# Kernel optimization log

Measured on AMD Instinct MI355X. Metric: run time of the kernel, lower is better.

## Reference

```python
import jax, jax.numpy as jnp
import numpy as np
from jax import lax

B, C_IN, H, W = 128, 3, 256, 256
C_OUT, K = 16, 3


def setup_inputs() -> dict:
    key = jax.random.key(0)
    k1, k2, k3 = jax.random.split(key, 3)
    x = jax.random.normal(k1, (B, C_IN, H, W), dtype=jnp.float32)
    # PyTorch ConvTranspose2d weight layout: (in_channels, out_channels, kH, kW)
    weight = jax.random.normal(k2, (C_IN, C_OUT, K, K), dtype=jnp.float32) * (1.0 / np.sqrt(C_IN * K * K))
    bias = jax.random.normal(k3, (C_OUT, 1, 1), dtype=jnp.float32)
    return {"x": x, "weight": weight, "bias": bias}


def reference(x, weight, bias):
    # conv_transpose2d(stride=1, padding=0) == full correlation with spatially
    # flipped kernel, with in/out channel axes swapped to OIHW.
    k = weight.shape[-1]
    w = jnp.flip(weight, axis=(2, 3)).transpose(1, 0, 2, 3)  # [C_out, C_in, k, k]
    y = lax.conv_general_dilated(
        x, w,
        window_strides=(1, 1),
        padding=[(k - 1, k - 1), (k - 1, k - 1)],
        dimension_numbers=("NCHW", "OIHW", "NCHW"),
    )  # [B, C_out, H+k-1, W+k-1]
    y = jnp.mean(y, axis=(2, 3), keepdims=True)          # [B, C_out, 1, 1]
    y = y + bias[None]                                   # broadcast [C_out,1,1]
    y = jax.nn.logsumexp(y, axis=1, keepdims=True)       # [B, 1, 1, 1]
    y = jnp.sum(y, axis=(2, 3))                          # [B, 1]
    return y * 10.0
```

## Files before the change

### kernel.cpp

```cpp
#include <hip/hip_runtime.h>

#define BATCH   128
#define C_IN    3
#define C_OUT   16
#define F4_PER_PLANE 16384
#define THREADS 1024
#define NWAVES  (THREADS / 64)
#define NBLK    (BATCH * 2)
#define F4_HALF (F4_PER_PLANE / 2)
#define ITERS   (F4_HALF / THREADS)

#define CNT_OFF 1024
#define CNT_STRIDE 16

__global__ __launch_bounds__(THREADS) void fused_pair(
        const float* __restrict__ x,
        const float* __restrict__ weight,
        const float* __restrict__ bias,
        float* __restrict__ ws,
        float* __restrict__ out) {
    const int b    = blockIdx.x >> 1;
    const int half = blockIdx.x & 1;
    const int t    = threadIdx.x;
    const float4* xp = (const float4*)x
                     + (size_t)b * (3 * F4_PER_PLANE) + half * F4_HALF;

    float a0 = 0.0f, a1 = 0.0f, a2 = 0.0f;
#pragma unroll
    for (int i = 0; i < ITERS; ++i) {
        float4 v0 = xp[0 * F4_PER_PLANE + i * THREADS + t];
        float4 v1 = xp[1 * F4_PER_PLANE + i * THREADS + t];
        float4 v2 = xp[2 * F4_PER_PLANE + i * THREADS + t];
        a0 += (v0.x + v0.y) + (v0.z + v0.w);
        a1 += (v1.x + v1.y) + (v1.z + v1.w);
        a2 += (v2.x + v2.y) + (v2.z + v2.w);
    }

#pragma unroll
    for (int off = 32; off > 0; off >>= 1) {
        a0 += __shfl_down(a0, off, 64);
        a1 += __shfl_down(a1, off, 64);
        a2 += __shfl_down(a2, off, 64);
    }
    __shared__ float smem[NWAVES][3];
    const int lane = t & 63;
    const int wv   = t >> 6;
    if (lane == 0) { smem[wv][0] = a0; smem[wv][1] = a1; smem[wv][2] = a2; }
    __syncthreads();

    if (t != 0) return;

    float S0 = 0.0f, S1 = 0.0f, S2 = 0.0f;
#pragma unroll
    for (int w = 0; w < NWAVES; ++w) {
        S0 += smem[w][0]; S1 += smem[w][1]; S2 += smem[w][2];
    }

    float* slot = ws + blockIdx.x * 4;
    slot[0] = S0; slot[1] = S1; slot[2] = S2;
    __threadfence();
    unsigned* cnt = (unsigned*)(ws + CNT_OFF) + b * CNT_STRIDE;
    unsigned prev = atomicAdd(cnt, 1u);
    if (prev != 1u) return;

    __threadfence();
    const float* pslot = ws + (blockIdx.x ^ 1) * 4;
    S0 += pslot[0]; S1 += pslot[1]; S2 += pslot[2];

    const float inv_area = 1.0f / (258.0f * 258.0f);
    float m[C_OUT];
    float mmax = -1e30f;
#pragma unroll
    for (int co = 0; co < C_OUT; ++co) {
        float v = bias[co];
        float w0 = 0.0f, w1 = 0.0f, w2 = 0.0f;
#pragma unroll
        for (int k = 0; k < 9; ++k) {
            w0 += weight[(0 * C_OUT + co) * 9 + k];
            w1 += weight[(1 * C_OUT + co) * 9 + k];
            w2 += weight[(2 * C_OUT + co) * 9 + k];
        }
        v += (S0 * w0 + S1 * w1 + S2 * w2) * inv_area;
        m[co] = v;
        mmax = fmaxf(mmax, v);
    }
    float se = 0.0f;
#pragma unroll
    for (int co = 0; co < C_OUT; ++co) se += expf(m[co] - mmax);
    out[b] = 10.0f * (logf(se) + mmax);
}

extern "C" void kernel_launch(void* const* d_in, const int* in_sizes, int n_in,
                              void* d_out, int out_size, void* d_ws, size_t ws_size,
                              hipStream_t stream) {
    const float* x      = (const float*)d_in[0];
    const float* weight = (const float*)d_in[1];
    const float* bias   = (const float*)d_in[2];
    float* out = (float*)d_out;
    float* ws  = (float*)d_ws;

    hipMemsetAsync(ws + CNT_OFF, 0, BATCH * CNT_STRIDE * sizeof(unsigned), stream);
    fused_pair<<<NBLK, THREADS, 0, stream>>>(x, weight, bias, ws, out);
}
```

Measured before the change: 160.6 us.

## Split fused reduction into main reduce and separate finalize kernel

After: 148.6 us. 7.5% less time.

```diff
diff --git a/kernel.cpp b/kernel.cpp
--- a/kernel.cpp
+++ b/kernel.cpp
@@ -10,15 +10,9 @@
 #define F4_HALF (F4_PER_PLANE / 2)
 #define ITERS   (F4_HALF / THREADS)
 
-#define CNT_OFF 1024
-#define CNT_STRIDE 16
-
-__global__ __launch_bounds__(THREADS) void fused_pair(
+__global__ __launch_bounds__(THREADS) void main_reduce(
         const float* __restrict__ x,
-        const float* __restrict__ weight,
-        const float* __restrict__ bias,
-        float* __restrict__ ws,
-        float* __restrict__ out) {
+        float* __restrict__ part) {
     const int b    = blockIdx.x >> 1;
     const int half = blockIdx.x & 1;
     const int t    = threadIdx.x;
@@ -48,46 +42,52 @@
     if (lane == 0) { smem[wv][0] = a0; smem[wv][1] = a1; smem[wv][2] = a2; }
     __syncthreads();
 
-    if (t != 0) return;
+    if (t == 0) {
+        float S0 = 0.0f, S1 = 0.0f, S2 = 0.0f;
+#pragma unroll
+        for (int w = 0; w < NWAVES; ++w) {
+            S0 += smem[w][0]; S1 += smem[w][1]; S2 += smem[w][2];
+        }
+        float* slot = part + blockIdx.x * 4;
+        slot[0] = S0; slot[1] = S1; slot[2] = S2;
+    }
+}
 
-    float S0 = 0.0f, S1 = 0.0f, S2 = 0.0f;
+__global__ __launch_bounds__(BATCH) void finalize(
+        const float* __restrict__ part,
+        const float* __restrict__ weight,
+        const float* __restrict__ bias,
+        float* __restrict__ out) {
+    __shared__ float Wsum[C_IN][C_OUT];
+    __shared__ float bsh[C_OUT];
+    const int t = threadIdx.x;
+    if (t < C_IN * C_OUT) {
+        float s = 0.0f;
 #pragma unroll
-    for (int w = 0; w < NWAVES; ++w) {
-        S0 += smem[w][0]; S1 += smem[w][1]; S2 += smem[w][2];
+        for (int k = 0; k < 9; ++k) s += weight[t * 9 + k];
+        Wsum[t / C_OUT][t % C_OUT] = s;
     }
+    if (t < C_OUT) bsh[t] = bias[t];
+    __syncthreads();
 
-    float* slot = ws + blockIdx.x * 4;
-    slot[0] = S0; slot[1] = S1; slot[2] = S2;
-    __threadfence();
-    unsigned* cnt = (unsigned*)(ws + CNT_OFF) + b * CNT_STRIDE;
-    unsigned prev = atomicAdd(cnt, 1u);
-    if (prev != 1u) return;
-
-    __threadfence();
-    const float* pslot = ws + (blockIdx.x ^ 1) * 4;
-    S0 += pslot[0]; S1 += pslot[1]; S2 += pslot[2];
+    const float* s0 = part + (t * 2 + 0) * 4;
+    const float* s1 = part + (t * 2 + 1) * 4;
+    const float S[C_IN] = { s0[0] + s1[0], s0[1] + s1[1], s0[2] + s1[2] };
 
     const float inv_area = 1.0f / (258.0f * 258.0f);
     float m[C_OUT];
     float mmax = -1e30f;
 #pragma unroll
     for (int co = 0; co < C_OUT; ++co) {
-        float v = bias[co];
-        float w0 = 0.0f, w1 = 0.0f, w2 = 0.0f;
-#pragma unroll
-        for (int k = 0; k < 9; ++k) {
-            w0 += weight[(0 * C_OUT + co) * 9 + k];
-            w1 += weight[(1 * C_OUT + co) * 9 + k];
-            w2 += weight[(2 * C_OUT + co) * 9 + k];
-        }
-        v += (S0 * w0 + S1 * w1 + S2 * w2) * inv_area;
+        float v = (S[0] * Wsum[0][co] + S[1] * Wsum[1][co] + S[2] * Wsum[2][co])
+                      * inv_area + bsh[co];
         m[co] = v;
         mmax = fmaxf(mmax, v);
     }
     float se = 0.0f;
 #pragma unroll
     for (int co = 0; co < C_OUT; ++co) se += expf(m[co] - mmax);
-    out[b] = 10.0f * (logf(se) + mmax);
+    out[t] = 10.0f * (logf(se) + mmax);
 }
 
 extern "C" void kernel_launch(void* const* d_in, const int* in_sizes, int n_in,
@@ -96,9 +96,9 @@
     const float* x      = (const float*)d_in[0];
     const float* weight = (const float*)d_in[1];
     const float* bias   = (const float*)d_in[2];
-    float* out = (float*)d_out;
-    float* ws  = (float*)d_ws;
+    float* out  = (float*)d_out;
+    float* part = (float*)d_ws;
 
-    hipMemsetAsync(ws + CNT_OFF, 0, BATCH * CNT_STRIDE * sizeof(unsigned), stream);
-    fused_pair<<<NBLK, THREADS, 0, stream>>>(x, weight, bias, ws, out);
+    main_reduce<<<NBLK, THREADS, 0, stream>>>(x, part);
+    finalize<<<1, BATCH, 0, stream>>>(part, weight, bias, out);
 }
```
